# Kernel tuning notes

Hardware: AMD Instinct MI355X
Metric: run time of the kernel (lower is better)

## Reference

```python
import jax, jax.numpy as jnp
import numpy as np

N = 20480    # total nodes in batched graph (64 graphs x 320 nodes)
E = 327680   # edges, avg in-degree 16
G = 64       # graphs in the batch
IN_DIM = 128
H = 4        # attention heads per layer
D = 64       # hidden dim per head (num_hidden)
C = 10       # num_classes
NEG_SLOPE = 0.2


def _gat_layer(h, src, dst, W, al, ar, residual):
    # DGL GATConv: fc -> per-head attention logits -> edge softmax over dst -> scatter-sum
    z = (h @ W).reshape(N, H, D)                       # [N,H,D]
    el = jnp.sum(z * al, axis=-1)                      # [N,H]
    er = jnp.sum(z * ar, axis=-1)                      # [N,H]
    e = jax.nn.leaky_relu(el[src] + er[dst], NEG_SLOPE)  # [E,H]
    m = jax.lax.stop_gradient(jax.ops.segment_max(e, dst, num_segments=N))
    m = jnp.where(jnp.isfinite(m), m, 0.0)
    ex = jnp.exp(e - m[dst])                           # [E,H]
    s = jax.ops.segment_sum(ex, dst, num_segments=N)   # [N,H]
    a = ex / jnp.where(s > 0, s, 1.0)[dst]             # [E,H] edge softmax
    msg = z[src] * a[:, :, None]                       # [E,H,D] (dominant intermediate)
    out = jax.ops.segment_sum(msg, dst, num_segments=N)  # [N,H,D]
    if residual:
        out = out + h.reshape(N, H, D)                 # res_fc is Identity (in == H*D)
        out = jax.nn.elu(out)                          # GATConv-internal activation
    return jax.nn.elu(out.reshape(N, H * D))           # model-level activation after flatten


def setup_inputs() -> dict:
    key = jax.random.key(0)
    ks = jax.random.split(key, 16)
    x = jax.random.normal(ks[0], (N, IN_DIM), jnp.float32)
    src = jax.random.randint(ks[1], (E,), 0, N, dtype=jnp.int32)
    # guarantee every node has >= 1 incoming edge (valid softmax denominator)
    dst = jnp.concatenate([jnp.arange(N, dtype=jnp.int32),
                           jax.random.randint(ks[2], (E - N,), 0, N, dtype=jnp.int32)])
    graph_ids = jnp.repeat(jnp.arange(G, dtype=jnp.int32), N // G)

    def lin(k, fi, fo):
        return (jax.random.normal(k, (fi, fo), jnp.float32) / np.float32(np.sqrt(fi)))

    def attn(k):
        return jax.random.normal(k, (H, D), jnp.float32) * np.float32(0.1)

    return {
        "x": x, "src": src, "dst": dst, "graph_ids": graph_ids,
        "W0": lin(ks[3], IN_DIM, H * D), "al0": attn(ks[4]), "ar0": attn(ks[5]),
        "W1": lin(ks[6], H * D, H * D), "al1": attn(ks[7]), "ar1": attn(ks[8]),
        "W2": lin(ks[9], H * D, H * D), "al2": attn(ks[10]), "ar2": attn(ks[11]),
        "Wc": lin(ks[12], H * D, C),
        "bc": jnp.zeros((C,), jnp.float32),
    }


def reference(x, src, dst, graph_ids, W0, al0, ar0, W1, al1, ar1, W2, al2, ar2, Wc, bc):
    h = _gat_layer(x, src, dst, W0, al0, ar0, residual=False)  # layer 0: no residual/act inside
    h = _gat_layer(h, src, dst, W1, al1, ar1, residual=True)
    h = _gat_layer(h, src, dst, W2, al2, ar2, residual=True)
    # dgl.mean_nodes: per-graph mean over node features
    hg = jax.ops.segment_sum(h, graph_ids, num_segments=G) / np.float32(N // G)  # [G, H*D]
    hg = jax.nn.elu(hg)
    return hg @ Wc + bc                                        # [G, C] logits
```

## Files before the change

### kernel.cpp

```cpp
#include <hip/hip_runtime.h>


#define NNODES 20480
#define NEDGES 327680
#define NGRAPH 64
#define NPG    320
#define HD     256
#define NH     4
#define NCLS   10
#define SLOTS  80

typedef __attribute__((ext_vector_type(8))) short short8;
typedef __attribute__((ext_vector_type(8))) unsigned short ushort8v;
typedef __attribute__((ext_vector_type(4))) float f32x4;

__device__ __forceinline__ float elu_f(float x)   { return x > 0.f ? x : expm1f(x); }
__device__ __forceinline__ float lrelu_f(float x) { return x > 0.f ? x : 0.2f * x; }

__device__ __forceinline__ ushort f2bf(float v) {
    uint u = __float_as_uint(v);
    uint r = (u + 0x7fffu + ((u >> 16) & 1u)) >> 16;
    return (ushort)r;
}
__device__ __forceinline__ float bf2f(ushort u) {
    return __uint_as_float(((uint)u) << 16);
}

__device__ __forceinline__ void split8(const float* __restrict__ p,
                                       short8& hi, short8& lo) {
    float4 a = *reinterpret_cast<const float4*>(p);
    float4 b = *reinterpret_cast<const float4*>(p + 4);
    float v[8] = {a.x, a.y, a.z, a.w, b.x, b.y, b.z, b.w};
    #pragma unroll
    for (int e = 0; e < 8; e++) {
        uint u = __float_as_uint(v[e]);
        hi[e] = (short)(u >> 16);
        float hf = __uint_as_float(u & 0xFFFF0000u);
        float lf = v[e] - hf;
        lo[e] = (short)(__float_as_uint(lf) >> 16);
    }
}

__global__ __launch_bounds__(256) void prep_k(
        const int* __restrict__ src, const int* __restrict__ dst,
        int* __restrict__ deg, int* __restrict__ slots,
        const float* __restrict__ W0, ushort* __restrict__ B0h, ushort* __restrict__ B0l,
        const float* __restrict__ W1, ushort* __restrict__ B1h, ushort* __restrict__ B1l,
        const float* __restrict__ W2, ushort* __restrict__ B2h, ushort* __restrict__ B2l) {
    int b = blockIdx.x;
    if (b < NEDGES / 256) {
        int e = b * 256 + threadIdx.x;
        int d = dst[e];
        int pos = atomicAdd(&deg[d], 1);
        if (pos < SLOTS) slots[d * SLOTS + pos] = src[e];
    } else {
        int idx = (b - NEDGES / 256) * 256 + threadIdx.x;
        const float* W; ushort *Bh, *Bl;
        if (idx < 128 * 256)          { W = W0; Bh = B0h; Bl = B0l; }
        else if (idx < 384 * 256)     { W = W1; Bh = B1h; Bl = B1l; idx -= 128 * 256; }
        else                          { W = W2; Bh = B2h; Bl = B2l; idx -= 384 * 256; }
        int k = idx >> 8, col = idx & 255;
        float v = W[idx];
        ushort h = f2bf(v);
        float vh = bf2f(h);
        ushort l = f2bf(v - vh);
        size_t o = (size_t)(k >> 5) * 8192 + (size_t)col * 32 + (k & 31);
        Bh[o] = h;
        Bl[o] = l;
    }
}

template<int ABF16>
__global__ __launch_bounds__(256) void gemm_mfma_k(
        const void* __restrict__ Av,
        const ushort* __restrict__ Bhi, const ushort* __restrict__ Blo,
        const float* __restrict__ al_, const float* __restrict__ ar_,
        ushort* __restrict__ zbf, float* __restrict__ el, float* __restrict__ er,
        int K) {
    int m0 = blockIdx.x * 32;
    int w = threadIdx.x >> 6, l = threadIdx.x & 63;
    int n0 = w * 64;
    int lr = l & 15, lk = l >> 4;
    f32x4 acc[2][4] = {};
    int ksteps = K >> 5;
    for (int kt = 0; kt < ksteps; kt++) {
        int kbase = kt * 32 + lk * 8;
        short8 a_hi[2], a_lo[2], b_hi[4], b_lo[4];
        #pragma unroll
        for (int i = 0; i < 2; i++) {
            size_t off = (size_t)(m0 + i * 16 + lr) * K + kbase;
            if (ABF16) {
                a_hi[i] = *reinterpret_cast<const short8*>((const ushort*)Av + off);
            } else {
                split8((const float*)Av + off, a_hi[i], a_lo[i]);
            }
        }
        #pragma unroll
        for (int j = 0; j < 4; j++) {
            size_t off = (size_t)kt * 8192 + (size_t)(n0 + j * 16 + lr) * 32 + lk * 8;
            b_hi[j] = *reinterpret_cast<const short8*>(Bhi + off);
            b_lo[j] = *reinterpret_cast<const short8*>(Blo + off);
        }
        #pragma unroll
        for (int i = 0; i < 2; i++)
            #pragma unroll
            for (int j = 0; j < 4; j++) {
                acc[i][j] = __builtin_amdgcn_mfma_f32_16x16x32_bf16(a_hi[i], b_hi[j], acc[i][j], 0, 0, 0);
                acc[i][j] = __builtin_amdgcn_mfma_f32_16x16x32_bf16(a_hi[i], b_lo[j], acc[i][j], 0, 0, 0);
                if (!ABF16)
                    acc[i][j] = __builtin_amdgcn_mfma_f32_16x16x32_bf16(a_lo[i], b_hi[j], acc[i][j], 0, 0, 0);
            }
    }
    float alv[4], arv[4];
    #pragma unroll
    for (int j = 0; j < 4; j++) {
        int col = n0 + j * 16 + lr;
        alv[j] = al_[col];
        arv[j] = ar_[col];
    }
    #pragma unroll
    for (int i = 0; i < 2; i++) {
        #pragma unroll
        for (int r = 0; r < 4; r++) {
            float pel = 0.f, per = 0.f;
            #pragma unroll
            for (int j = 0; j < 4; j++) {
                float v = acc[i][j][r];
                pel += v * alv[j];
                per += v * arv[j];
                int row = m0 + i * 16 + lk * 4 + r;
                int col = n0 + j * 16 + lr;
                zbf[(size_t)row * HD + col] = f2bf(v);
            }
            #pragma unroll
            for (int off = 1; off < 16; off <<= 1) {
                pel += __shfl_xor(pel, off);
                per += __shfl_xor(per, off);
            }
            if (lr == 0) {
                int row = m0 + i * 16 + lk * 4 + r;
                el[row * NH + w] = pel;
                er[row * NH + w] = per;
            }
        }
    }
}

__global__ __launch_bounds__(256) void attn_aggr_k(
        const ushort* __restrict__ zbf,
        const float* __restrict__ el, const float* __restrict__ er,
        const int* __restrict__ deg, const int* __restrict__ slots,
        const ushort* __restrict__ hin, ushort* __restrict__ hout,
        int residual) {
    int wid = threadIdx.x >> 6, lane = threadIdx.x & 63;
    int n = blockIdx.x * 4 + wid;
    int h = lane >> 4, j16 = lane & 15;
    int l32 = lane & 31, half = lane >> 5;
    int headL = l32 >> 3;
    int col8 = l32 * 8;
    int d = deg[n];
    if (d > SLOTS) d = SLOTS;
    const int* sl = slots + (size_t)n * SLOTS;
    float ern = er[n * NH + h];
    float acc[8] = {};

    if (d <= 64) {
        float pv[4];
        int   sv[4];
        #pragma unroll
        for (int u = 0; u < 4; u++) {
            int k = u * 16 + j16;
            if (k < d) {
                sv[u] = sl[k];
                pv[u] = __expf(lrelu_f(el[sv[u] * NH + h] + ern));
            } else {
                sv[u] = 0;
                pv[u] = 0.f;
            }
        }
        float ssum = pv[0] + pv[1] + pv[2] + pv[3];
        #pragma unroll
        for (int off = 1; off < 16; off <<= 1) ssum += __shfl_xor(ssum, off);
        float rinv = 1.f / ssum;
        #pragma unroll
        for (int u = 0; u < 4; u++) pv[u] *= rinv;
        #pragma unroll
        for (int u = 0; u < 4; u++) {
            if (u * 16 >= d) break;
            #pragma unroll
            for (int jj = 0; jj < 8; jj++) {
                int e = u * 16 + jj * 2 + half;
                int srcl = headL * 16 + jj * 2 + half;
                float w = __shfl(pv[u], srcl);
                int   s = __shfl(sv[u], srcl);
                if (e < d) {
                    ushort8v zv = *reinterpret_cast<const ushort8v*>(&zbf[(size_t)s * HD + col8]);
                    #pragma unroll
                    for (int t = 0; t < 8; t++) acc[t] += bf2f(zv[t]) * w;
                }
            }
        }
        #pragma unroll
        for (int t = 0; t < 8; t++) acc[t] += __shfl_xor(acc[t], 32);
    } else {
        float ssum = 0.f;
        for (int k = j16; k < d; k += 16)
            ssum += __expf(lrelu_f(el[sl[k] * NH + h] + ern));
        #pragma unroll
        for (int off = 1; off < 16; off <<= 1) ssum += __shfl_xor(ssum, off);
        float rinv = 1.f / ssum;
        float rinvL = __shfl(rinv, headL * 16);
        float ernL = er[n * NH + headL];
        for (int k = 0; k < d; k++) {
            int s = sl[k];
            float w = __expf(lrelu_f(el[s * NH + headL] + ernL)) * rinvL;
            ushort8v zv = *reinterpret_cast<const ushort8v*>(&zbf[(size_t)s * HD + col8]);
            #pragma unroll
            for (int t = 0; t < 8; t++) acc[t] += bf2f(zv[t]) * w;
        }
    }

    if (half == 0) {
        size_t o = (size_t)n * HD + col8;
        ushort8v r;
        if (residual) {
            ushort8v hv = *reinterpret_cast<const ushort8v*>(&hin[o]);
            #pragma unroll
            for (int t = 0; t < 8; t++)
                r[t] = f2bf(elu_f(elu_f(acc[t] + bf2f(hv[t]))));
        } else {
            #pragma unroll
            for (int t = 0; t < 8; t++)
                r[t] = f2bf(elu_f(acc[t]));
        }
        *reinterpret_cast<ushort8v*>(&hout[o]) = r;
    }
}

__global__ __launch_bounds__(1024) void poolcls_k(const ushort* __restrict__ h,
                                                  const float* __restrict__ Wc,
                                                  const float* __restrict__ bc,
                                                  float* __restrict__ out) {
    __shared__ float part[4][HD];
    __shared__ float hv[HD];
    int g = blockIdx.x, t = threadIdx.x;
    int col = t & 255, q = t >> 8;
    const ushort* p = h + (size_t)g * NPG * HD + (size_t)q * (NPG / 4) * HD + col;
    float s = 0.f;
    for (int i = 0; i < NPG / 4; i++) s += bf2f(p[(size_t)i * HD]);
    part[q][col] = s;
    __syncthreads();
    if (t < HD) {
        float tot = part[0][t] + part[1][t] + part[2][t] + part[3][t];
        hv[t] = elu_f(tot * (1.0f / NPG));
    }
    __syncthreads();
    if (t < NCLS) {
        float acc = bc[t];
        for (int k = 0; k < HD; k++) acc += hv[k] * Wc[k * NCLS + t];
        out[g * NCLS + t] = acc;
    }
}

extern "C" void kernel_launch(void* const* d_in, const int* in_sizes, int n_in,
                              void* d_out, int out_size, void* d_ws, size_t ws_size,
                              hipStream_t stream) {
    const float* x   = (const float*)d_in[0];
    const int*   src = (const int*)d_in[1];
    const int*   dst = (const int*)d_in[2];
    const float* W0  = (const float*)d_in[4];
    const float* al0 = (const float*)d_in[5];
    const float* ar0 = (const float*)d_in[6];
    const float* W1  = (const float*)d_in[7];
    const float* al1 = (const float*)d_in[8];
    const float* ar1 = (const float*)d_in[9];
    const float* W2  = (const float*)d_in[10];
    const float* al2 = (const float*)d_in[11];
    const float* ar2 = (const float*)d_in[12];
    const float* Wc  = (const float*)d_in[13];
    const float* bc  = (const float*)d_in[14];
    float* out = (float*)d_out;

    char* ws = (char*)d_ws;
    size_t off = 0;
    auto alloc = [&](size_t bytes) -> void* {
        void* p = ws + off;
        off = (off + bytes + 255) & ~(size_t)255;
        return p;
    };
    ushort* hbuf     = (ushort*)alloc((size_t)NNODES * HD * 2);
    ushort* zbf      = (ushort*)alloc((size_t)NNODES * HD * 2);
    float*  el       = (float*)alloc((size_t)NNODES * NH * 4);
    float*  er       = (float*)alloc((size_t)NNODES * NH * 4);
    int*    deg      = (int*)alloc((size_t)NNODES * 4);
    int*    slots    = (int*)alloc((size_t)NNODES * SLOTS * 4);
    ushort* B0h      = (ushort*)alloc((size_t)128 * 256 * 2);
    ushort* B0l      = (ushort*)alloc((size_t)128 * 256 * 2);
    ushort* B1h      = (ushort*)alloc((size_t)256 * 256 * 2);
    ushort* B1l      = (ushort*)alloc((size_t)256 * 256 * 2);
    ushort* B2h      = (ushort*)alloc((size_t)256 * 256 * 2);
    ushort* B2l      = (ushort*)alloc((size_t)256 * 256 * 2);

    hipMemsetAsync(deg, 0, (size_t)NNODES * 4, stream);
    prep_k<<<NEDGES / 256 + (128 + 256 + 256), 256, 0, stream>>>(
        src, dst, deg, slots,
        W0, B0h, B0l, W1, B1h, B1l, W2, B2h, B2l);

    gemm_mfma_k<0><<<NNODES / 32, 256, 0, stream>>>(x, B0h, B0l, al0, ar0,
                                                    zbf, el, er, 128);
    attn_aggr_k<<<NNODES / 4, 256, 0, stream>>>(zbf, el, er, deg, slots,
                                                nullptr, hbuf, 0);
    gemm_mfma_k<1><<<NNODES / 32, 256, 0, stream>>>(hbuf, B1h, B1l, al1, ar1,
                                                    zbf, el, er, 256);
    attn_aggr_k<<<NNODES / 4, 256, 0, stream>>>(zbf, el, er, deg, slots,
                                                hbuf, hbuf, 1);
    gemm_mfma_k<1><<<NNODES / 32, 256, 0, stream>>>(hbuf, B2h, B2l, al2, ar2,
                                                    zbf, el, er, 256);
    attn_aggr_k<<<NNODES / 4, 256, 0, stream>>>(zbf, el, er, deg, slots,
                                                hbuf, hbuf, 1);

    poolcls_k<<<NGRAPH, 1024, 0, stream>>>(hbuf, Wc, bc, out);
}
```

Measured before the change: 275.4 us.

## Fuse attention aggregation with next layer's GEMM via shared-memory tile

Replaces the separate aggregation and GEMM kernels for layers 1 and 2 with a fused kernel. Each 512-thread block aggregates 32 destination nodes, writes the activated rows to hbuf and to a swizzled LDS tile, then runs the next layer's MFMA GEMM from LDS and emits z, el and er. Ping-pong z/el/er buffers avoid read-write hazards across blocks. This removes two launches and the global re-read of h for the GEMM. In exchange the per-block aggregation is serialized over 4 rows per wave, and the GEMM phase uses only 32-row tiles, which may hurt occupancy and latency hiding. The layer-0 GEMM is specialized with K fixed at 128 and the loop fully unrolled.

```diff
diff --git a/kernel.cpp b/kernel.cpp
--- a/kernel.cpp
+++ b/kernel.cpp
@@ -70,30 +70,25 @@
     }
 }
 
-template<int ABF16>
-__global__ __launch_bounds__(256) void gemm_mfma_k(
-        const void* __restrict__ Av,
+__global__ __launch_bounds__(256) void gemm0_k(
+        const float* __restrict__ A,
         const ushort* __restrict__ Bhi, const ushort* __restrict__ Blo,
         const float* __restrict__ al_, const float* __restrict__ ar_,
-        ushort* __restrict__ zbf, float* __restrict__ el, float* __restrict__ er,
-        int K) {
+        ushort* __restrict__ zbf, float* __restrict__ el, float* __restrict__ er) {
+    const int K = 128;
     int m0 = blockIdx.x * 32;
     int w = threadIdx.x >> 6, l = threadIdx.x & 63;
     int n0 = w * 64;
     int lr = l & 15, lk = l >> 4;
     f32x4 acc[2][4] = {};
-    int ksteps = K >> 5;
-    for (int kt = 0; kt < ksteps; kt++) {
+    #pragma unroll
+    for (int kt = 0; kt < K / 32; kt++) {
         int kbase = kt * 32 + lk * 8;
         short8 a_hi[2], a_lo[2], b_hi[4], b_lo[4];
         #pragma unroll
         for (int i = 0; i < 2; i++) {
             size_t off = (size_t)(m0 + i * 16 + lr) * K + kbase;
-            if (ABF16) {
-                a_hi[i] = *reinterpret_cast<const short8*>((const ushort*)Av + off);
-            } else {
-                split8((const float*)Av + off, a_hi[i], a_lo[i]);
-            }
+            split8(A + off, a_hi[i], a_lo[i]);
         }
         #pragma unroll
         for (int j = 0; j < 4; j++) {
@@ -107,8 +102,7 @@
             for (int j = 0; j < 4; j++) {
                 acc[i][j] = __builtin_amdgcn_mfma_f32_16x16x32_bf16(a_hi[i], b_hi[j], acc[i][j], 0, 0, 0);
                 acc[i][j] = __builtin_amdgcn_mfma_f32_16x16x32_bf16(a_hi[i], b_lo[j], acc[i][j], 0, 0, 0);
-                if (!ABF16)
-                    acc[i][j] = __builtin_amdgcn_mfma_f32_16x16x32_bf16(a_lo[i], b_hi[j], acc[i][j], 0, 0, 0);
+                acc[i][j] = __builtin_amdgcn_mfma_f32_16x16x32_bf16(a_lo[i], b_hi[j], acc[i][j], 0, 0, 0);
             }
     }
     float alv[4], arv[4];
@@ -234,6 +228,157 @@
                 r[t] = f2bf(elu_f(acc[t]));
         }
         *reinterpret_cast<ushort8v*>(&hout[o]) = r;
+    }
+}
+
+template<int RES>
+__global__ __launch_bounds__(512) void attn_gemm_k(
+        const ushort* __restrict__ zin,
+        const float* __restrict__ eli, const float* __restrict__ eri,
+        const int* __restrict__ deg, const int* __restrict__ slots,
+        ushort* __restrict__ hbuf,
+        const ushort* __restrict__ Bhi, const ushort* __restrict__ Blo,
+        const float* __restrict__ al_, const float* __restrict__ ar_,
+        ushort* __restrict__ zout, float* __restrict__ elo, float* __restrict__ ero) {
+    __shared__ ushort hts[32 * 256];
+    int m0 = blockIdx.x * 32;
+    int wv = threadIdx.x >> 6, lane = threadIdx.x & 63;
+    int h = lane >> 4, j16 = lane & 15;
+    int l32 = lane & 31, half = lane >> 5;
+    int headL = l32 >> 3;
+    int col8 = l32 * 8;
+
+    for (int q = 0; q < 4; q++) {
+        int rloc = wv * 4 + q;
+        int n = m0 + rloc;
+        int d = deg[n];
+        if (d > SLOTS) d = SLOTS;
+        const int* sl = slots + (size_t)n * SLOTS;
+        float ern = eri[n * NH + h];
+        float acc[8] = {};
+
+        if (d <= 64) {
+            float pv[4];
+            int   sv[4];
+            #pragma unroll
+            for (int u = 0; u < 4; u++) {
+                int k = u * 16 + j16;
+                if (k < d) {
+                    sv[u] = sl[k];
+                    pv[u] = __expf(lrelu_f(eli[sv[u] * NH + h] + ern));
+                } else {
+                    sv[u] = 0;
+                    pv[u] = 0.f;
+                }
+            }
+            float ssum = pv[0] + pv[1] + pv[2] + pv[3];
+            #pragma unroll
+            for (int off = 1; off < 16; off <<= 1) ssum += __shfl_xor(ssum, off);
+            float rinv = 1.f / ssum;
+            #pragma unroll
+            for (int u = 0; u < 4; u++) pv[u] *= rinv;
+            #pragma unroll
+            for (int u = 0; u < 4; u++) {
+                if (u * 16 >= d) break;
+                #pragma unroll
+                for (int jj = 0; jj < 8; jj++) {
+                    int e = u * 16 + jj * 2 + half;
+                    int srcl = headL * 16 + jj * 2 + half;
+                    float w = __shfl(pv[u], srcl);
+                    int   s = __shfl(sv[u], srcl);
+                    if (e < d) {
+                        ushort8v zv = *reinterpret_cast<const ushort8v*>(&zin[(size_t)s * HD + col8]);
+                        #pragma unroll
+                        for (int t = 0; t < 8; t++) acc[t] += bf2f(zv[t]) * w;
+                    }
+                }
+            }
+            #pragma unroll
+            for (int t = 0; t < 8; t++) acc[t] += __shfl_xor(acc[t], 32);
+        } else {
+            float ssum = 0.f;
+            for (int k = j16; k < d; k += 16)
+                ssum += __expf(lrelu_f(eli[sl[k] * NH + h] + ern));
+            #pragma unroll
+            for (int off = 1; off < 16; off <<= 1) ssum += __shfl_xor(ssum, off);
+            float rinv = 1.f / ssum;
+            float rinvL = __shfl(rinv, headL * 16);
+            float ernL = eri[n * NH + headL];
+            for (int k = 0; k < d; k++) {
+                int s = sl[k];
+                float w = __expf(lrelu_f(eli[s * NH + headL] + ernL)) * rinvL;
+                ushort8v zv = *reinterpret_cast<const ushort8v*>(&zin[(size_t)s * HD + col8]);
+                #pragma unroll
+                for (int t = 0; t < 8; t++) acc[t] += bf2f(zv[t]) * w;
+            }
+        }
+
+        if (half == 0) {
+            size_t o = (size_t)n * HD + col8;
+            ushort8v r;
+            if (RES) {
+                ushort8v hv = *reinterpret_cast<const ushort8v*>(&hbuf[o]);
+                #pragma unroll
+                for (int t = 0; t < 8; t++)
+                    r[t] = f2bf(elu_f(elu_f(acc[t] + bf2f(hv[t]))));
+            } else {
+                #pragma unroll
+                for (int t = 0; t < 8; t++)
+                    r[t] = f2bf(elu_f(acc[t]));
+            }
+            *reinterpret_cast<ushort8v*>(&hbuf[o]) = r;
+            *reinterpret_cast<ushort8v*>(&hts[rloc * 256 + (col8 ^ ((rloc & 7) << 3))]) = r;
+        }
+    }
+    __syncthreads();
+
+    int wr = wv >> 2, wc = wv & 3;
+    int n0 = wc * 64;
+    int lr = lane & 15, lk = lane >> 4;
+    f32x4 gacc[4] = {};
+    #pragma unroll
+    for (int kt = 0; kt < 8; kt++) {
+        int arow = wr * 16 + lr;
+        short8 a = *reinterpret_cast<const short8*>(
+            &hts[arow * 256 + ((((kt * 4 + lk) ^ (arow & 7)) << 3))]);
+        #pragma unroll
+        for (int j = 0; j < 4; j++) {
+            size_t off = (size_t)kt * 8192 + (size_t)(n0 + j * 16 + lr) * 32 + lk * 8;
+            short8 bh = *reinterpret_cast<const short8*>(Bhi + off);
+            short8 bl = *reinterpret_cast<const short8*>(Blo + off);
+            gacc[j] = __builtin_amdgcn_mfma_f32_16x16x32_bf16(a, bh, gacc[j], 0, 0, 0);
+            gacc[j] = __builtin_amdgcn_mfma_f32_16x16x32_bf16(a, bl, gacc[j], 0, 0, 0);
+        }
+    }
+    float alv[4], arv[4];
+    #pragma unroll
+    for (int j = 0; j < 4; j++) {
+        int col = n0 + j * 16 + lr;
+        alv[j] = al_[col];
+        arv[j] = ar_[col];
+    }
+    #pragma unroll
+    for (int r = 0; r < 4; r++) {
+        float pel = 0.f, per = 0.f;
+        #pragma unroll
+        for (int j = 0; j < 4; j++) {
+            float v = gacc[j][r];
+            pel += v * alv[j];
+            per += v * arv[j];
+            int row = m0 + wr * 16 + lk * 4 + r;
+            int col = n0 + j * 16 + lr;
+            zout[(size_t)row * HD + col] = f2bf(v);
+        }
+        #pragma unroll
+        for (int off = 1; off < 16; off <<= 1) {
+            pel += __shfl_xor(pel, off);
+            per += __shfl_xor(per, off);
+        }
+        if (lr == 0) {
+            int row = m0 + wr * 16 + lk * 4 + r;
+            elo[row * NH + wc] = pel;
+            ero[row * NH + wc] = per;
+        }
     }
 }
 
@@ -289,9 +434,12 @@
         return p;
     };
     ushort* hbuf     = (ushort*)alloc((size_t)NNODES * HD * 2);
-    ushort* zbf      = (ushort*)alloc((size_t)NNODES * HD * 2);
-    float*  el       = (float*)alloc((size_t)NNODES * NH * 4);
-    float*  er       = (float*)alloc((size_t)NNODES * NH * 4);
+    ushort* zA       = (ushort*)alloc((size_t)NNODES * HD * 2);
+    ushort* zB       = (ushort*)alloc((size_t)NNODES * HD * 2);
+    float*  elA      = (float*)alloc((size_t)NNODES * NH * 4);
+    float*  erA      = (float*)alloc((size_t)NNODES * NH * 4);
+    float*  elB      = (float*)alloc((size_t)NNODES * NH * 4);
+    float*  erB      = (float*)alloc((size_t)NNODES * NH * 4);
     int*    deg      = (int*)alloc((size_t)NNODES * 4);
     int*    slots    = (int*)alloc((size_t)NNODES * SLOTS * 4);
     ushort* B0h      = (ushort*)alloc((size_t)128 * 256 * 2);
@@ -306,18 +454,16 @@
         src, dst, deg, slots,
         W0, B0h, B0l, W1, B1h, B1l, W2, B2h, B2l);
 
-    gemm_mfma_k<0><<<NNODES / 32, 256, 0, stream>>>(x, B0h, B0l, al0, ar0,
-                                                    zbf, el, er, 128);
-    attn_aggr_k<<<NNODES / 4, 256, 0, stream>>>(zbf, el, er, deg, slots,
-                                                nullptr, hbuf, 0);
-    gemm_mfma_k<1><<<NNODES / 32, 256, 0, stream>>>(hbuf, B1h, B1l, al1, ar1,
-                                                    zbf, el, er, 256);
-    attn_aggr_k<<<NNODES / 4, 256, 0, stream>>>(zbf, el, er, deg, slots,
+    gemm0_k<<<NNODES / 32, 256, 0, stream>>>(x, B0h, B0l, al0, ar0, zA, elA, erA);
+
+    attn_gemm_k<0><<<NNODES / 32, 512, 0, stream>>>(
+        zA, elA, erA, deg, slots, hbuf, B1h, B1l, al1, ar1, zB, elB, erB);
+
+    attn_gemm_k<1><<<NNODES / 32, 512, 0, stream>>>(
+        zB, elB, erB, deg, slots, hbuf, B2h, B2l, al2, ar2, zA, elA, erA);
+
+    attn_aggr_k<<<NNODES / 4, 256, 0, stream>>>(zA, elA, erA, deg, slots,
                                                 hbuf, hbuf, 1);
-    gemm_mfma_k<1><<<NNODES / 32, 256, 0, stream>>>(hbuf, B2h, B2l, al2, ar2,
-                                                    zbf, el, er, 256);
-    attn_aggr_k<<<NNODES / 4, 256, 0, stream>>>(zbf, el, er, deg, slots,
-                                                hbuf, hbuf, 1);
 
     poolcls_k<<<NGRAPH, 1024, 0, stream>>>(hbuf, Wc, bc, out);
 }
```

Result: slower. 315.0 us (+14.4%).
